# Performance work log

Measured on AMD Instinct MI355X. Metric: run time of the kernel, lower is better.

## Reference

```python
import jax, jax.numpy as jnp
import numpy as np
import math

B, S, H, DM = 1, 2048, 16, 1024
DK = DM // H
MAX_SEQ = 2048  # rel_embed has MAX_SEQ+1 rows


def setup_inputs() -> dict:
    rng = jax.random.key(0)
    ks = jax.random.split(rng, 12)
    w = lambda k, shape, s=0.02: (jax.random.normal(k, shape, jnp.float32) * s)
    inp = {
        'query': jax.random.normal(ks[0], (B, S, DM), jnp.float32),
        'key':   jax.random.normal(ks[1], (B, S, DM), jnp.float32),
        'value': jax.random.normal(ks[2], (B, S, DM), jnp.float32),
        # causal integer mask [B,S,S] (cumsum over it derives rel-pos indices)
        'mask': jnp.broadcast_to(jnp.tril(jnp.ones((S, S), jnp.int32)), (B, S, S)),
        'Wq': w(ks[3], (DM, DM)), 'bq': jnp.zeros((DM,), jnp.float32),
        'Wk': w(ks[4], (DM, DM)), 'bk': jnp.zeros((DM,), jnp.float32),
        'Wv': w(ks[5], (DM, DM)), 'bv': jnp.zeros((DM,), jnp.float32),
        'Wo': w(ks[6], (DM, DM)), 'bo': jnp.zeros((DM,), jnp.float32),
        # relative position embeddings [h, max_seq_len+1, d_k], N(0,1) as in the module
        'rel_embed': jax.random.normal(ks[7], (H, MAX_SEQ + 1, DK), jnp.float32),
    }
    return inp


def reference(query, key, value, mask, Wq, bq, Wk, bk, Wv, bv, Wo, bo, rel_embed):
    scale = 1.0 / math.sqrt(DK)
    heads = lambda x, W, b: (x @ W.T + b).reshape(B, S, H, DK).transpose(0, 2, 1, 3)
    q = heads(query, Wq, bq)   # [B,H,S,DK]
    k = heads(key, Wk, bk)
    v = heads(value, Wv, bv)

    scores = jnp.einsum('bhid,bhjd->bhij', q, k) * scale  # [B,H,S,S]

    m4 = mask[:, None, :, :]                 # [B,1,S,S]
    nz = m4 != 0
    # torch: cumsum(mask)-1 picks the m-index; index 0 (then zeroed) where mask==0
    m_idx = jnp.where(nz, jnp.cumsum(m4, axis=-1) - 1, 0)  # [B,1,S,S]

    # rel_scores[b,h,m,l] = <q[b,h,l,:], rel_embed[h,m,:]> / sqrt(d_k)
    rel = jnp.einsum('bhld,hmd->bhml', q, rel_embed[:, :S]) * scale  # [B,H,S,S]
    idx = jnp.broadcast_to(m_idx, (B, H, S, S))
    # torch.take flat-index decodes to rel[b,h, m_idx[i,j], j]
    rel_g = jnp.take_along_axis(rel, idx, axis=2) * nz.astype(scores.dtype)

    scores = jnp.where(nz, scores + rel_g, jnp.float32(-1e9))
    p = jax.nn.softmax(scores, axis=-1)      # dropout p=0.0 -> identity

    out = jnp.einsum('bhij,bhjd->bhid', p, v)         # [B,H,S,DK]
    out = out.transpose(0, 2, 1, 3).reshape(B, S, DM)  # [B,S,DM]
    return out @ Wo.T + bo
```

## Files before the change

### kernel.cpp

```cpp
#include <hip/hip_runtime.h>

typedef __bf16 bf16_t;
typedef __bf16 bf16x4 __attribute__((ext_vector_type(4)));
typedef __bf16 bf16x8 __attribute__((ext_vector_type(8)));
typedef float  f32x4  __attribute__((ext_vector_type(4)));
typedef float  f32x16 __attribute__((ext_vector_type(16)));
typedef unsigned int u32;

#define S_LEN 2048
#define DMODEL 1024
#define NHEAD 16
#define DHEAD 64
#define RELROWS 2049

__device__ __forceinline__ void gload16(const void* g, void* l) {
    __builtin_amdgcn_global_load_lds((const __attribute__((address_space(1))) void*)g,
                                     (__attribute__((address_space(3))) void*)l,
                                     16, 0, 0);
}

__device__ __forceinline__ f32x4 mfma16(bf16x8 a, bf16x8 b, f32x4 c) {
    return __builtin_amdgcn_mfma_f32_16x16x32_bf16(a, b, c, 0, 0, 0);
}
__device__ __forceinline__ f32x16 mfma32(bf16x8 a, bf16x8 b, f32x16 c) {
    return __builtin_amdgcn_mfma_f32_32x32x16_bf16(a, b, c, 0, 0, 0);
}

__device__ __forceinline__ bf16x8 lds_read_swz(const bf16_t* base, int row, int colb) {
    return *(const bf16x8*)((const char*)base + row * 128 + (colb ^ ((row & 7) << 4)));
}

__device__ __forceinline__ u32 cvtpk(float lo, float hi) {
    u32 w;
    asm("v_cvt_pk_bf16_f32 %0, %1, %2" : "=v"(w) : "v"(lo), "v"(hi));
    return w;
}
__device__ __forceinline__ void swap32(u32& a, u32& b) {
    asm("v_permlane32_swap_b32 %0, %1" : "+v"(a), "+v"(b));
}

__global__ __launch_bounds__(256)
void f2bf_all(const float* __restrict__ xq, const float* __restrict__ xk,
              const float* __restrict__ xv,
              const float* __restrict__ wq, const float* __restrict__ wk,
              const float* __restrict__ wv, const float* __restrict__ wo,
              bf16_t* __restrict__ dst, int n4X, int n4W) {
    const int i = blockIdx.x * blockDim.x + threadIdx.x;
    const float* src; int j;
    if (i < 3 * n4X) {
        if (i < n4X)            { src = xq; j = i; }
        else if (i < 2 * n4X)   { src = xk; j = i - n4X; }
        else                    { src = xv; j = i - 2 * n4X; }
    } else {
        int w = i - 3 * n4X;
        if (w < n4W)            { src = wq; j = w; }
        else if (w < 2 * n4W)   { src = wk; j = w - n4W; }
        else if (w < 3 * n4W)   { src = wv; j = w - 2 * n4W; }
        else                    { src = wo; j = w - 3 * n4W; }
    }
    float4 v = ((const float4*)src)[j];
    bf16x4 o;
    o[0] = (bf16_t)v.x; o[1] = (bf16_t)v.y; o[2] = (bf16_t)v.z; o[3] = (bf16_t)v.w;
    ((bf16x4*)dst)[i] = o;
}

template <int MODE, int BM, int BN>
__global__ __launch_bounds__(256)
void gemm_bt(const bf16_t* __restrict__ Abase, const bf16_t* __restrict__ Wbase,
             const float* __restrict__ b0, const float* __restrict__ b1,
             const float* __restrict__ b2,
             bf16_t* __restrict__ outb, float* __restrict__ outf,
             int M, int N, int K) {
    __shared__ alignas(16) bf16_t As[2][BM * 64];
    __shared__ alignas(16) bf16_t Bs[2][BN * 64];
    const int tid = threadIdx.x, lane = tid & 63, wave = tid >> 6;
    const int z = blockIdx.z;
    const bf16_t* A = Abase + (size_t)z * M * K;
    const bf16_t* W = Wbase + (size_t)z * N * K;
    const float* bias = (z == 0) ? b0 : (z == 1 ? b1 : b2);
    const int nwg = gridDim.x * gridDim.y;
    const int wg = blockIdx.y * gridDim.x + blockIdx.x;
    const int swz = (wg & 7) * (nwg >> 3) + (wg >> 3);
    const int m0 = (swz / gridDim.x) * BM, n0 = (swz % gridDim.x) * BN;
    const int wr = (wave >> 1) * (BM / 2), wc = (wave & 1) * (BN / 2);
    constexpr int MR = BM / 32, NR = BN / 32;
    constexpr int LOADS = BM / 32 + BN / 32;

    f32x4 acc[MR][NR] = {};
    const int soff = wave * 1024 + lane * 16;

    auto stage = [&](int b, int kt) {
#pragma unroll
        for (int r = 0; r < BM / 32; ++r) {
            int e = (r * 4096 + soff) >> 1;
            int row = e >> 6, col = e & 63;
            gload16(A + (size_t)(m0 + row) * K + kt + col,
                    (char*)As[b] + r * 4096 + wave * 1024);
        }
#pragma unroll
        for (int r = 0; r < BN / 32; ++r) {
            int e = (r * 4096 + soff) >> 1;
            int row = e >> 6, col = e & 63;
            gload16(W + (size_t)(n0 + row) * K + kt + col,
                    (char*)Bs[b] + r * 4096 + wave * 1024);
        }
    };

    const int NK = K >> 6;
    stage(0, 0);
    for (int s = 0; s < NK; ++s) {
        const int buf = s & 1;
        if (s + 1 < NK) {
            stage(buf ^ 1, (s + 1) << 6);
            if constexpr (LOADS == 6) asm volatile("s_waitcnt vmcnt(6)" ::: "memory");
            else if constexpr (LOADS == 4) asm volatile("s_waitcnt vmcnt(4)" ::: "memory");
            else asm volatile("s_waitcnt vmcnt(8)" ::: "memory");
        } else {
            asm volatile("s_waitcnt vmcnt(0)" ::: "memory");
        }
        asm volatile("s_barrier" ::: "memory");
#pragma unroll
        for (int kk = 0; kk < 2; ++kk) {
            bf16x8 af[MR], bfr[NR];
#pragma unroll
            for (int m = 0; m < MR; ++m)
                af[m] = *(const bf16x8*)&As[buf][(wr + m * 16 + (lane & 15)) * 64 + kk * 32 + (lane >> 4) * 8];
#pragma unroll
            for (int n = 0; n < NR; ++n)
                bfr[n] = *(const bf16x8*)&Bs[buf][(wc + n * 16 + (lane & 15)) * 64 + kk * 32 + (lane >> 4) * 8];
#pragma unroll
            for (int m = 0; m < MR; ++m)
#pragma unroll
                for (int n = 0; n < NR; ++n)
                    acc[m][n] = mfma16(af[m], bfr[n], acc[m][n]);
        }
        asm volatile("s_barrier" ::: "memory");
    }

    const float scale = (MODE == 0 && z == 0) ? 0.125f : 1.0f;
#pragma unroll
    for (int m = 0; m < MR; ++m) {
        const int gi = m0 + wr + m * 16 + (lane >> 4) * 4;
#pragma unroll
        for (int n = 0; n < NR; ++n) {
            const int gj = n0 + wc + n * 16 + (lane & 15);
            const float bv = bias[gj];
#pragma unroll
            for (int r2 = 0; r2 < 4; ++r2) {
                float v = (acc[m][n][r2] + bv) * scale;
                if (MODE == 0)
                    outb[(size_t)z * M * N + (size_t)(gi + r2) * N + gj] = (bf16_t)v;
                else
                    outf[(size_t)(gi + r2) * N + gj] = v;
            }
        }
    }
}

__global__ __launch_bounds__(256)
void prep_v(const bf16_t* __restrict__ Qb, const float* __restrict__ rel,
            const bf16_t* __restrict__ V,
            bf16_t* __restrict__ Vtp, float* __restrict__ RG) {
    __shared__ float t[64][65];
    const int s0 = blockIdx.x * 64, h = blockIdx.y;
    const int tid = threadIdx.x;
    {
        const int j = tid >> 2, dq = tid & 3;
        const bf16_t* qp = Qb + (size_t)(s0 + j) * DMODEL + h * DHEAD + dq * 16;
        const float* rp = rel + ((size_t)h * RELROWS + (s0 + j)) * DHEAD + dq * 16;
        bf16x8 q0 = *(const bf16x8*)qp;
        bf16x8 q1 = *(const bf16x8*)(qp + 8);
        float4 r0 = *(const float4*)(rp + 0), r1 = *(const float4*)(rp + 4);
        float4 r2 = *(const float4*)(rp + 8), r3 = *(const float4*)(rp + 12);
        float acc = 0.f;
        acc += (float)q0[0] * r0.x + (float)q0[1] * r0.y + (float)q0[2] * r0.z + (float)q0[3] * r0.w;
        acc += (float)q0[4] * r1.x + (float)q0[5] * r1.y + (float)q0[6] * r1.z + (float)q0[7] * r1.w;
        acc += (float)q1[0] * r2.x + (float)q1[1] * r2.y + (float)q1[2] * r2.z + (float)q1[3] * r2.w;
        acc += (float)q1[4] * r3.x + (float)q1[5] * r3.y + (float)q1[6] * r3.z + (float)q1[7] * r3.w;
        acc += __shfl_xor(acc, 1);
        acc += __shfl_xor(acc, 2);
        if (dq == 0) RG[h * S_LEN + s0 + j] = acc;
    }
#pragma unroll
    for (int it = 0; it < 16; ++it) {
        int idx = it * 256 + tid;
        int r = idx >> 6, c = idx & 63;
        t[r][c] = (float)V[(size_t)(s0 + r) * DMODEL + h * DHEAD + c];
    }
    __syncthreads();
#pragma unroll
    for (int it = 0; it < 16; ++it) {
        int idx = it * 256 + tid;
        int r = idx >> 6, c = idx & 63;
        Vtp[(size_t)(h * DHEAD + r) * S_LEN + s0 + c] = (bf16_t)t[c][r];
    }
}

__global__ __launch_bounds__(256, 2)
void flash_attn(const bf16_t* __restrict__ Qb, const bf16_t* __restrict__ Kb,
                const bf16_t* __restrict__ Vtp, const float* __restrict__ RG,
                bf16_t* __restrict__ Ob) {
    __shared__ alignas(16) bf16_t KB[4][64 * 64];
    __shared__ alignas(16) bf16_t VB[4][64 * 64];
    __shared__ alignas(16) bf16_t Qs[64 * 64];
    __shared__ alignas(16) float Rs[S_LEN];
    const int tid = threadIdx.x, lane = tid & 63, wave = tid >> 6;
    const int qt = (int)gridDim.x - 1 - (int)blockIdx.x;
    const int h = blockIdx.y;
    const int q0 = qt * 64;
    const int nt = qt + 1;
    const int lo5 = lane & 31, hi = lane >> 5;
    const int qhalf = wave & 1;
    const int par = wave >> 1;

    const int nkv = nt * 64;
    if (tid * 8 < nkv) {
        float4 a = *(const float4*)&RG[h * S_LEN + tid * 8];
        float4 b = *(const float4*)&RG[h * S_LEN + tid * 8 + 4];
        *(float4*)&Rs[tid * 8] = a;
        *(float4*)&Rs[tid * 8 + 4] = b;
    }

    auto stage_tile = [&](int tt) {
        const int bse = tt & 3;
#pragma unroll
        for (int r2 = 0; r2 < 2; ++r2) {
            int rr = wave * 2 + r2;
            int L = rr * 1024 + lane * 16;
            int row = L >> 7, colb = (L & 127) ^ ((row & 7) << 4);
            gload16(Kb + (size_t)(tt * 64 + row) * DMODEL + h * DHEAD + (colb >> 1),
                    (char*)KB[bse] + rr * 1024);
            gload16(Vtp + (size_t)(h * DHEAD + row) * S_LEN + tt * 64 + (colb >> 1),
                    (char*)VB[bse] + rr * 1024);
        }
    };

#pragma unroll
    for (int r2 = 0; r2 < 2; ++r2) {
        int rr = wave * 2 + r2;
        int L = rr * 1024 + lane * 16;
        int row = L >> 7, colb = (L & 127) ^ ((row & 7) << 4);
        gload16(Qb + (size_t)(q0 + row) * DMODEL + h * DHEAD + (colb >> 1),
                (char*)Qs + rr * 1024);
    }
    stage_tile(0);
    stage_tile(nt > 1 ? 1 : 0);
    asm volatile("s_waitcnt vmcnt(8) lgkmcnt(0)\n\ts_barrier" ::: "memory");

    bf16x8 qf[4];
#pragma unroll
    for (int c = 0; c < 4; ++c)
        qf[c] = lds_read_swz(Qs, qhalf * 32 + lo5, c * 32 + hi * 16);

    f32x16 oacc[2] = {};
    float ls = 0.f;

    for (int t2 = 0; t2 < nt; t2 += 2) {
        if (t2 + 3 < nt) {
            stage_tile(t2 + 2);
            stage_tile(t2 + 3);
            asm volatile("s_waitcnt vmcnt(8)\n\ts_barrier" ::: "memory");
        } else if (t2 + 2 < nt) {
            stage_tile(t2 + 2);
            asm volatile("s_waitcnt vmcnt(4)\n\ts_barrier" ::: "memory");
        } else {
            asm volatile("s_waitcnt vmcnt(0)\n\ts_barrier" ::: "memory");
        }

        const int tt = t2 + par;
        if (tt < nt) {
            const int buf = tt & 3;
            const int kv0 = tt * 64;
            const bool diag = (tt == nt - 1);
            u32 pw[4][4];
#pragma unroll
            for (int kb = 0; kb < 2; ++kb) {
                f32x16 st;
#pragma unroll
                for (int g = 0; g < 4; ++g) {
                    f32x4 rv = *(const f32x4*)&Rs[kv0 + kb * 32 + g * 8 + hi * 4];
#pragma unroll
                    for (int e = 0; e < 4; ++e) st[g * 4 + e] = rv[e];
                }
                __builtin_amdgcn_s_setprio(1);
#pragma unroll
                for (int c = 0; c < 4; ++c) {
                    bf16x8 kf = lds_read_swz(KB[buf], kb * 32 + lo5, c * 32 + hi * 16);
                    st = mfma32(kf, qf[c], st);
                }
                __builtin_amdgcn_s_setprio(0);
                float pr[16];
                if (diag) {
#pragma unroll
                    for (int r = 0; r < 16; ++r) {
                        int kloc = kb * 32 + (r & 3) + 8 * (r >> 2) + 4 * hi;
                        float v = __expf(st[r]);
                        pr[r] = (kloc > qhalf * 32 + lo5) ? 0.f : v;
                    }
                } else {
#pragma unroll
                    for (int r = 0; r < 16; ++r) pr[r] = __expf(st[r]);
                }
#pragma unroll
                for (int r = 0; r < 16; ++r) ls += pr[r];
#pragma unroll
                for (int hf = 0; hf < 2; ++hf) {
                    u32 a  = cvtpk(pr[8 * hf + 0], pr[8 * hf + 1]);
                    u32 b  = cvtpk(pr[8 * hf + 4], pr[8 * hf + 5]);
                    swap32(a, b);
                    u32 c2 = cvtpk(pr[8 * hf + 2], pr[8 * hf + 3]);
                    u32 d2 = cvtpk(pr[8 * hf + 6], pr[8 * hf + 7]);
                    swap32(c2, d2);
                    pw[kb * 2 + hf][0] = a;  pw[kb * 2 + hf][1] = c2;
                    pw[kb * 2 + hf][2] = b;  pw[kb * 2 + hf][3] = d2;
                }
            }
            __builtin_amdgcn_s_setprio(1);
#pragma unroll
            for (int kc = 0; kc < 4; ++kc) {
                union { u32 w[4]; bf16x8 v; } uu;
                uu.w[0] = pw[kc][0]; uu.w[1] = pw[kc][1]; uu.w[2] = pw[kc][2]; uu.w[3] = pw[kc][3];
#pragma unroll
                for (int db = 0; db < 2; ++db) {
                    bf16x8 vf = lds_read_swz(VB[buf], db * 32 + lo5, kc * 32 + hi * 16);
                    oacc[db] = mfma32(vf, uu.v, oacc[db]);
                }
            }
            __builtin_amdgcn_s_setprio(0);
        }
        asm volatile("s_barrier" ::: "memory");
    }

    asm volatile("s_waitcnt vmcnt(0)" ::: "memory");
    if (wave >= 2) {
        char* base = (char*)KB[0] + (wave - 2) * 9728 + lane * 144;
#pragma unroll
        for (int db = 0; db < 2; ++db)
#pragma unroll
            for (int g = 0; g < 4; ++g) {
                f32x4 v4;
#pragma unroll
                for (int e = 0; e < 4; ++e) v4[e] = oacc[db][g * 4 + e];
                *(f32x4*)(base + (db * 4 + g) * 16) = v4;
            }
        *(float*)((char*)KB[0] + 19456 + (wave - 2) * 256 + lane * 4) = ls;
    }
    __syncthreads();
    if (wave < 2) {
        const char* base = (const char*)KB[0] + wave * 9728 + lane * 144;
#pragma unroll
        for (int db = 0; db < 2; ++db)
#pragma unroll
            for (int g = 0; g < 4; ++g) {
                f32x4 v4 = *(const f32x4*)(base + (db * 4 + g) * 16);
#pragma unroll
                for (int e = 0; e < 4; ++e) oacc[db][g * 4 + e] += v4[e];
            }
        ls += *(const float*)((const char*)KB[0] + 19456 + wave * 256 + lane * 4);
        ls += __shfl_xor(ls, 32);
        const float inv = 1.0f / ls;
        const int qg = q0 + wave * 32 + lo5;
#pragma unroll
        for (int db = 0; db < 2; ++db)
#pragma unroll
            for (int g = 0; g < 4; ++g) {
                bf16x4 o4;
#pragma unroll
                for (int e = 0; e < 4; ++e)
                    o4[e] = (bf16_t)(oacc[db][g * 4 + e] * inv);
                *(bf16x4*)&Ob[(size_t)qg * DMODEL + h * DHEAD + db * 32 + g * 8 + hi * 4] = o4;
            }
    }
}

extern "C" void kernel_launch(void* const* d_in, const int* in_sizes, int n_in,
                              void* d_out, int out_size, void* d_ws, size_t ws_size,
                              hipStream_t stream) {
    const float* query = (const float*)d_in[0];
    const float* key   = (const float*)d_in[1];
    const float* value = (const float*)d_in[2];
    const float* Wq  = (const float*)d_in[4];
    const float* bq  = (const float*)d_in[5];
    const float* Wk  = (const float*)d_in[6];
    const float* bk  = (const float*)d_in[7];
    const float* Wv  = (const float*)d_in[8];
    const float* bv  = (const float*)d_in[9];
    const float* Wo  = (const float*)d_in[10];
    const float* bo  = (const float*)d_in[11];
    const float* rel = (const float*)d_in[12];

    char* ws = (char*)d_ws;
    const size_t nX = (size_t)S_LEN * DMODEL;
    const size_t nW = (size_t)DMODEL * DMODEL;
    bf16_t* Xbf  = (bf16_t*)ws;
    bf16_t* Wbf  = (bf16_t*)(ws + 3 * nX * 2);
    bf16_t* QKV  = (bf16_t*)(ws + 3 * nX * 2 + 4 * nW * 2);
    bf16_t* Vtp  = (bf16_t*)ws;
    bf16_t* AOb  = (bf16_t*)(ws + nX * 2);
    float*  RG   = (float*)(ws + 2 * nX * 2);
    (void)in_sizes; (void)n_in; (void)out_size; (void)ws_size;

    const int n4X = (int)(nX / 4), n4W = (int)(nW / 4);
    const int tot4 = 3 * n4X + 4 * n4W;
    f2bf_all<<<tot4 / 256, 256, 0, stream>>>(query, key, value, Wq, Wk, Wv, Wo,
                                             Xbf, n4X, n4W);

    gemm_bt<0, 128, 64><<<dim3(DMODEL / 64, S_LEN / 128, 3), 256, 0, stream>>>(
        Xbf, Wbf, bq, bk, bv, QKV, nullptr, S_LEN, DMODEL, DMODEL);

    prep_v<<<dim3(S_LEN / 64, NHEAD), 256, 0, stream>>>(QKV, rel, QKV + 2 * nX, Vtp, RG);
    flash_attn<<<dim3(S_LEN / 64, NHEAD), 256, 0, stream>>>(QKV, QKV + nX, Vtp, RG, AOb);

    gemm_bt<1, 64, 64><<<dim3(DMODEL / 64, S_LEN / 64, 1), 256, 0, stream>>>(
        AOb, Wbf + 3 * nW, bo, bo, bo, nullptr, (float*)d_out, S_LEN, DMODEL, DMODEL);
}
```

Measured before the change: 89.63 us.

## Fuse rel-diagonal dot and V transpose into QKV GEMM epilogue; interleave score halves

Removes the separate prep_v kernel. The QKV GEMM epilogue now writes V directly in transposed layout and computes the per-row relative-position dot product (Q·rel) for the Q slice, reducing it with shuffles and LDS. In flash_attn, both 32-key score blocks are computed back to back before the exp and pack step, giving more independent MFMA work to overlap. This saves one launch and a re-read of Q and V, but adds strided 8-byte transposed stores and extra fp32 rel loads to the GEMM epilogue.

```diff
diff --git a/kernel.cpp b/kernel.cpp
--- a/kernel.cpp
+++ b/kernel.cpp
@@ -70,6 +70,8 @@
              const float* __restrict__ b0, const float* __restrict__ b1,
              const float* __restrict__ b2,
              bf16_t* __restrict__ outb, float* __restrict__ outf,
+             const float* __restrict__ relp, float* __restrict__ RGout,
+             bf16_t* __restrict__ vtp,
              int M, int N, int K) {
     __shared__ alignas(16) bf16_t As[2][BM * 64];
     __shared__ alignas(16) bf16_t Bs[2][BN * 64];
@@ -138,6 +140,14 @@
     }
 
     const float scale = (MODE == 0 && z == 0) ? 0.125f : 1.0f;
+    float rp[MR][4];
+    if constexpr (MODE == 0) {
+#pragma unroll
+        for (int m = 0; m < MR; ++m)
+#pragma unroll
+            for (int r2 = 0; r2 < 4; ++r2) rp[m][r2] = 0.f;
+    }
+    const int hh = n0 >> 6;
 #pragma unroll
     for (int m = 0; m < MR; ++m) {
         const int gi = m0 + wr + m * 16 + (lane >> 4) * 4;
@@ -145,54 +155,49 @@
         for (int n = 0; n < NR; ++n) {
             const int gj = n0 + wc + n * 16 + (lane & 15);
             const float bv = bias[gj];
-#pragma unroll
-            for (int r2 = 0; r2 < 4; ++r2) {
-                float v = (acc[m][n][r2] + bv) * scale;
-                if (MODE == 0)
-                    outb[(size_t)z * M * N + (size_t)(gi + r2) * N + gj] = (bf16_t)v;
-                else
-                    outf[(size_t)(gi + r2) * N + gj] = v;
-            }
-        }
-    }
-}
-
-__global__ __launch_bounds__(256)
-void prep_v(const bf16_t* __restrict__ Qb, const float* __restrict__ rel,
-            const bf16_t* __restrict__ V,
-            bf16_t* __restrict__ Vtp, float* __restrict__ RG) {
-    __shared__ float t[64][65];
-    const int s0 = blockIdx.x * 64, h = blockIdx.y;
-    const int tid = threadIdx.x;
-    {
-        const int j = tid >> 2, dq = tid & 3;
-        const bf16_t* qp = Qb + (size_t)(s0 + j) * DMODEL + h * DHEAD + dq * 16;
-        const float* rp = rel + ((size_t)h * RELROWS + (s0 + j)) * DHEAD + dq * 16;
-        bf16x8 q0 = *(const bf16x8*)qp;
-        bf16x8 q1 = *(const bf16x8*)(qp + 8);
-        float4 r0 = *(const float4*)(rp + 0), r1 = *(const float4*)(rp + 4);
-        float4 r2 = *(const float4*)(rp + 8), r3 = *(const float4*)(rp + 12);
-        float acc = 0.f;
-        acc += (float)q0[0] * r0.x + (float)q0[1] * r0.y + (float)q0[2] * r0.z + (float)q0[3] * r0.w;
-        acc += (float)q0[4] * r1.x + (float)q0[5] * r1.y + (float)q0[6] * r1.z + (float)q0[7] * r1.w;
-        acc += (float)q1[0] * r2.x + (float)q1[1] * r2.y + (float)q1[2] * r2.z + (float)q1[3] * r2.w;
-        acc += (float)q1[4] * r3.x + (float)q1[5] * r3.y + (float)q1[6] * r3.z + (float)q1[7] * r3.w;
-        acc += __shfl_xor(acc, 1);
-        acc += __shfl_xor(acc, 2);
-        if (dq == 0) RG[h * S_LEN + s0 + j] = acc;
-    }
-#pragma unroll
-    for (int it = 0; it < 16; ++it) {
-        int idx = it * 256 + tid;
-        int r = idx >> 6, c = idx & 63;
-        t[r][c] = (float)V[(size_t)(s0 + r) * DMODEL + h * DHEAD + c];
-    }
-    __syncthreads();
-#pragma unroll
-    for (int it = 0; it < 16; ++it) {
-        int idx = it * 256 + tid;
-        int r = idx >> 6, c = idx & 63;
-        Vtp[(size_t)(h * DHEAD + r) * S_LEN + s0 + c] = (bf16_t)t[c][r];
+            if constexpr (MODE == 0) {
+                if (z == 2) {
+                    bf16x4 o4;
+#pragma unroll
+                    for (int r2 = 0; r2 < 4; ++r2) o4[r2] = (bf16_t)(acc[m][n][r2] + bv);
+                    *(bf16x4*)&vtp[(size_t)gj * S_LEN + gi] = o4;
+                } else {
+#pragma unroll
+                    for (int r2 = 0; r2 < 4; ++r2) {
+                        float v = (acc[m][n][r2] + bv) * scale;
+                        outb[(size_t)z * M * N + (size_t)(gi + r2) * N + gj] = (bf16_t)v;
+                        if (z == 0)
+                            rp[m][r2] += v * relp[((size_t)hh * RELROWS + (gi + r2)) * DHEAD + (gj & 63)];
+                    }
+                }
+            } else {
+#pragma unroll
+                for (int r2 = 0; r2 < 4; ++r2)
+                    outf[(size_t)(gi + r2) * N + gj] = acc[m][n][r2] + bv;
+            }
+        }
+    }
+    if constexpr (MODE == 0) {
+        if (z == 0) {
+            float* Rp = (float*)As;
+#pragma unroll
+            for (int m = 0; m < MR; ++m)
+#pragma unroll
+                for (int r2 = 0; r2 < 4; ++r2) {
+                    float p = rp[m][r2];
+                    p += __shfl_xor(p, 1);
+                    p += __shfl_xor(p, 2);
+                    p += __shfl_xor(p, 4);
+                    p += __shfl_xor(p, 8);
+                    if ((lane & 15) == 0)
+                        Rp[wave * 64 + m * 16 + (lane >> 4) * 4 + r2] = p;
+                }
+            __syncthreads();
+            if ((wave & 1) == 0) {
+                float v = Rp[wave * 64 + lane] + Rp[(wave + 1) * 64 + lane];
+                RGout[hh * S_LEN + m0 + wr + lane] = v;
+            }
+        }
     }
 }
 
@@ -272,48 +277,61 @@
             const int buf = tt & 3;
             const int kv0 = tt * 64;
             const bool diag = (tt == nt - 1);
+            f32x16 sta, stb;
+#pragma unroll
+            for (int g = 0; g < 4; ++g) {
+                f32x4 ra = *(const f32x4*)&Rs[kv0 + g * 8 + hi * 4];
+                f32x4 rb = *(const f32x4*)&Rs[kv0 + 32 + g * 8 + hi * 4];
+#pragma unroll
+                for (int e = 0; e < 4; ++e) { sta[g * 4 + e] = ra[e]; stb[g * 4 + e] = rb[e]; }
+            }
+            __builtin_amdgcn_s_setprio(1);
+#pragma unroll
+            for (int c = 0; c < 4; ++c) {
+                bf16x8 kfa = lds_read_swz(KB[buf], lo5, c * 32 + hi * 16);
+                sta = mfma32(kfa, qf[c], sta);
+            }
+#pragma unroll
+            for (int c = 0; c < 4; ++c) {
+                bf16x8 kfb = lds_read_swz(KB[buf], 32 + lo5, c * 32 + hi * 16);
+                stb = mfma32(kfb, qf[c], stb);
+            }
+            __builtin_amdgcn_s_setprio(0);
+            float pra[16], prb[16];
+            if (diag) {
+#pragma unroll
+                for (int r = 0; r < 16; ++r) {
+                    int kloc = (r & 3) + 8 * (r >> 2) + 4 * hi;
+                    float va = __expf(sta[r]), vb = __expf(stb[r]);
+                    pra[r] = (kloc > qhalf * 32 + lo5) ? 0.f : va;
+                    prb[r] = (kloc + 32 > qhalf * 32 + lo5) ? 0.f : vb;
+                }
+            } else {
+#pragma unroll
+                for (int r = 0; r < 16; ++r) { pra[r] = __expf(sta[r]); prb[r] = __expf(stb[r]); }
+            }
+#pragma unroll
+            for (int r = 0; r < 16; ++r) ls += pra[r] + prb[r];
             u32 pw[4][4];
 #pragma unroll
-            for (int kb = 0; kb < 2; ++kb) {
-                f32x16 st;
-#pragma unroll
-                for (int g = 0; g < 4; ++g) {
-                    f32x4 rv = *(const f32x4*)&Rs[kv0 + kb * 32 + g * 8 + hi * 4];
-#pragma unroll
-                    for (int e = 0; e < 4; ++e) st[g * 4 + e] = rv[e];
-                }
-                __builtin_amdgcn_s_setprio(1);
-#pragma unroll
-                for (int c = 0; c < 4; ++c) {
-                    bf16x8 kf = lds_read_swz(KB[buf], kb * 32 + lo5, c * 32 + hi * 16);
-                    st = mfma32(kf, qf[c], st);
-                }
-                __builtin_amdgcn_s_setprio(0);
-                float pr[16];
-                if (diag) {
-#pragma unroll
-                    for (int r = 0; r < 16; ++r) {
-                        int kloc = kb * 32 + (r & 3) + 8 * (r >> 2) + 4 * hi;
-                        float v = __expf(st[r]);
-                        pr[r] = (kloc > qhalf * 32 + lo5) ? 0.f : v;
-                    }
-                } else {
-#pragma unroll
-                    for (int r = 0; r < 16; ++r) pr[r] = __expf(st[r]);
-                }
-#pragma unroll
-                for (int r = 0; r < 16; ++r) ls += pr[r];
-#pragma unroll
-                for (int hf = 0; hf < 2; ++hf) {
-                    u32 a  = cvtpk(pr[8 * hf + 0], pr[8 * hf + 1]);
-                    u32 b  = cvtpk(pr[8 * hf + 4], pr[8 * hf + 5]);
-                    swap32(a, b);
-                    u32 c2 = cvtpk(pr[8 * hf + 2], pr[8 * hf + 3]);
-                    u32 d2 = cvtpk(pr[8 * hf + 6], pr[8 * hf + 7]);
-                    swap32(c2, d2);
-                    pw[kb * 2 + hf][0] = a;  pw[kb * 2 + hf][1] = c2;
-                    pw[kb * 2 + hf][2] = b;  pw[kb * 2 + hf][3] = d2;
-                }
+            for (int hf = 0; hf < 2; ++hf) {
+                u32 a  = cvtpk(pra[8 * hf + 0], pra[8 * hf + 1]);
+                u32 b  = cvtpk(pra[8 * hf + 4], pra[8 * hf + 5]);
+                swap32(a, b);
+                u32 c2 = cvtpk(pra[8 * hf + 2], pra[8 * hf + 3]);
+                u32 d2 = cvtpk(pra[8 * hf + 6], pra[8 * hf + 7]);
+                swap32(c2, d2);
+                pw[hf][0] = a;  pw[hf][1] = c2;  pw[hf][2] = b;  pw[hf][3] = d2;
+            }
+#pragma unroll
+            for (int hf = 0; hf < 2; ++hf) {
+                u32 a  = cvtpk(prb[8 * hf + 0], prb[8 * hf + 1]);
+                u32 b  = cvtpk(prb[8 * hf + 4], prb[8 * hf + 5]);
+                swap32(a, b);
+                u32 c2 = cvtpk(prb[8 * hf + 2], prb[8 * hf + 3]);
+                u32 d2 = cvtpk(prb[8 * hf + 6], prb[8 * hf + 7]);
+                swap32(c2, d2);
+                pw[2 + hf][0] = a;  pw[2 + hf][1] = c2;  pw[2 + hf][2] = b;  pw[2 + hf][3] = d2;
             }
             __builtin_amdgcn_s_setprio(1);
 #pragma unroll
@@ -395,9 +413,9 @@
     bf16_t* Xbf  = (bf16_t*)ws;
     bf16_t* Wbf  = (bf16_t*)(ws + 3 * nX * 2);
     bf16_t* QKV  = (bf16_t*)(ws + 3 * nX * 2 + 4 * nW * 2);
-    bf16_t* Vtp  = (bf16_t*)ws;
+    float*  RG   = (float*)(ws + 3 * nX * 2 + 4 * nW * 2 + 3 * nX * 2);
+    bf16_t* Vtp  = QKV + 2 * nX;
     bf16_t* AOb  = (bf16_t*)(ws + nX * 2);
-    float*  RG   = (float*)(ws + 2 * nX * 2);
     (void)in_sizes; (void)n_in; (void)out_size; (void)ws_size;
 
     const int n4X = (int)(nX / 4), n4W = (int)(nW / 4);
@@ -406,11 +424,11 @@
                                              Xbf, n4X, n4W);
 
     gemm_bt<0, 128, 64><<<dim3(DMODEL / 64, S_LEN / 128, 3), 256, 0, stream>>>(
-        Xbf, Wbf, bq, bk, bv, QKV, nullptr, S_LEN, DMODEL, DMODEL);
-
-    prep_v<<<dim3(S_LEN / 64, NHEAD), 256, 0, stream>>>(QKV, rel, QKV + 2 * nX, Vtp, RG);
+        Xbf, Wbf, bq, bk, bv, QKV, nullptr, rel, RG, Vtp, S_LEN, DMODEL, DMODEL);
+
     flash_attn<<<dim3(S_LEN / 64, NHEAD), 256, 0, stream>>>(QKV, QKV + nX, Vtp, RG, AOb);
 
     gemm_bt<1, 64, 64><<<dim3(DMODEL / 64, S_LEN / 64, 1), 256, 0, stream>>>(
-        AOb, Wbf + 3 * nW, bo, bo, bo, nullptr, (float*)d_out, S_LEN, DMODEL, DMODEL);
-}
+        AOb, Wbf + 3 * nW, bo, bo, bo, nullptr, (float*)d_out,
+        nullptr, nullptr, nullptr, S_LEN, DMODEL, DMODEL);
+}
```

Measured after the change: 89.71 us. About the same (+0.1%).
